# Kernel optimization log

Measured on AMD Instinct MI355X. Metric: run time of the kernel, lower is better.

Reference implementation:

```python
import jax, jax.numpy as jnp
import numpy as np

ALPHA = 0.5  # init alpha
B, T, D, H = 32, 1024, 512, 512


def _cell(x, h, c, wih, whh, bih, bhh):
    # PyTorch LSTM cell: gates in i, f, g, o order
    g = x @ wih.T + bih + h @ whh.T + bhh  # (B, 4H)
    i, f, gg, o = jnp.split(g, 4, axis=-1)
    c2 = jax.nn.sigmoid(f) * c + jax.nn.sigmoid(i) * jnp.tanh(gg)
    h2 = jax.nn.sigmoid(o) * jnp.tanh(c2)
    return h2, c2


def setup_inputs() -> dict:
    key = jax.random.key(0)
    ks = jax.random.split(key, 9)
    s = 1.0 / np.sqrt(H)  # torch default init scale
    u = lambda k, shp: jax.random.uniform(k, shp, jnp.float32, -s, s)
    return {
        "u_sequence": jax.random.normal(ks[0], (B, T, D), jnp.float32),
        "w_ih_f": u(ks[1], (4 * H, D)),
        "w_hh_f": u(ks[2], (4 * H, H)),
        "b_ih_f": u(ks[3], (4 * H,)),
        "b_hh_f": u(ks[4], (4 * H,)),
        "w_ih_b": u(ks[5], (4 * H, D)),
        "w_hh_b": u(ks[6], (4 * H, H)),
        "b_ih_b": u(ks[7], (4 * H,)),
        "b_hh_b": u(ks[8], (4 * H,)),
    }


def reference(u_sequence, w_ih_f, w_hh_f, b_ih_f, b_hh_f,
              w_ih_b, w_hh_b, b_ih_b, b_hh_b):
    # Per timestep the original calls the bidirectional LSTM on a length-1
    # slice: both directions reduce to a single cell step on the same input.
    # Hidden/cell state (2, B, H) is carried across timesteps.
    pf = (w_ih_f, w_hh_f, b_ih_f, b_hh_f)
    pb = (w_ih_b, w_hh_b, b_ih_b, b_hh_b)
    Bn, Tn, Dn = u_sequence.shape
    Hn = w_hh_f.shape[1]
    z = jnp.zeros((Bn, Hn), u_sequence.dtype)

    def bi_step(x, hf, cf, hb, cb):
        hf2, cf2 = _cell(x, hf, cf, *pf)
        hb2, cb2 = _cell(x, hb, cb, *pb)
        # lstm_out[:, 0, :] == concat(h_fwd, h_bwd) for seq_len == 1
        return jnp.concatenate([hf2, hb2], axis=-1), hf2, cf2, hb2, cb2

    def step(carry, u_t):  # u_t: (B, D)
        hf, cf, hb, cb = carry
        out1, hf1, cf1, hb1, cb1 = bi_step(u_t, hf, cf, hb, cb)
        x_hat = out1[:, -1:]                 # last channel scalar, (B, 1)
        x_hat_prime = u_t + x_hat            # broadcast -> (B, D)
        out2, hf2, cf2, hb2, cb2 = bi_step(x_hat_prime, hf1, cf1, hb1, cb1)
        x_hat_next = out2[:, -1:]
        out = u_t + (1.0 - ALPHA) * x_hat_prime + ALPHA * x_hat_next
        return (hf2, cf2, hb2, cb2), out

    u_tm = jnp.swapaxes(u_sequence, 0, 1)    # (T, B, D)
    _, outs = jax.lax.scan(step, (z, z, z, z), u_tm)
    return jnp.swapaxes(outs, 0, 1)          # (B, T, D)
```

## Files before the change

kernel.cpp:

```cpp
#include <hip/hip_runtime.h>
#include <cstdint>
#include <cstddef>

#define BB 32
#define TT 1024
#define DD 512
#define HH 512
#define NBLK 128

typedef __bf16 bf16x8 __attribute__((ext_vector_type(8)));
typedef float  f32x4  __attribute__((ext_vector_type(4)));
typedef unsigned long long u64;

#define HFRAG_OFF 0
#define XHAT_OFF  131072
#define XS_OFF    393216
#define FLAGS_OFF 655360

#define AT_LOAD(p)     __hip_atomic_load((p),      __ATOMIC_RELAXED, __HIP_MEMORY_SCOPE_AGENT)
#define AT_STORE(p, v) __hip_atomic_store((p), (v), __ATOMIC_RELAXED, __HIP_MEMORY_SCOPE_AGENT)

__device__ __forceinline__ float sigm(float x) {
    return 1.f / (1.f + __expf(-x));
}
__device__ __forceinline__ float tanh_fast(float x) {
    x = fminf(15.f, fmaxf(-15.f, x));
    float e = __expf(2.f * x);
    return (e - 1.f) / (e + 1.f);
}

__device__ __forceinline__ void barrier_arrive(int* flags, int bid, int n) {
    __builtin_amdgcn_s_waitcnt(0);
    __syncthreads();
    if (threadIdx.x == 0) AT_STORE(&flags[bid], n);
}
__device__ __forceinline__ void barrier_wait(const int* flags, int dir, int n) {
    if (threadIdx.x < 64) {
        const u64* f64 = (const u64*)(flags + (dir << 6));
        const int i = threadIdx.x & 31;
        for (;;) {
            u64 a = AT_LOAD(&f64[i]);
            bool ok = ((int)a >= n) & ((int)(a >> 32) >= n);
            if (__all(ok)) break;
            __builtin_amdgcn_s_sleep(1);
        }
    }
    __syncthreads();
}

__global__ __launch_bounds__(256, 1) void lstm_persistent(
    const float* __restrict__ u,
    const float* __restrict__ wih_f, const float* __restrict__ whh_f,
    const float* __restrict__ bih_f, const float* __restrict__ bhh_f,
    const float* __restrict__ wih_b, const float* __restrict__ whh_b,
    const float* __restrict__ bih_b, const float* __restrict__ bhh_b,
    unsigned short* __restrict__ hfrag, float* __restrict__ xhat,
    u64* __restrict__ xs, int* __restrict__ flags)
{
    const int bid  = blockIdx.x;
    const int dir  = bid >> 6;
    const int kb   = bid & 63;
    const int k0   = kb << 3;
    const int tid  = threadIdx.x;
    const int wid  = tid >> 6;
    const int mi   = wid >> 1;
    const int ni   = wid & 1;
    const int lane = tid & 63;
    const int quad = lane >> 4;
    const int l16  = lane & 15;

    const float* wih = dir ? wih_b : wih_f;
    const float* whh = dir ? whh_b : whh_f;
    const float* bih = dir ? bih_b : bih_f;
    const float* bhh = dir ? bhh_b : bhh_f;

    bf16x8 wihF[16], whhF[16];
    {
        const int jg = (l16 >> 2) * HH + (k0 + 4 * mi) + (l16 & 3);
        #pragma unroll
        for (int s = 0; s < 16; ++s) {
            const float* p = wih + (size_t)jg * DD + s * 32 + quad * 8;
            const float* q = whh + (size_t)jg * HH + s * 32 + quad * 8;
            bf16x8 a, b;
            #pragma unroll
            for (int i = 0; i < 8; ++i) { a[i] = (__bf16)p[i]; b[i] = (__bf16)q[i]; }
            wihF[s] = a;
            whhF[s] = b;
        }
    }

    const int kc = k0 + 4 * mi + quad;
    const int bc = ni * 16 + l16;

    float rsv[4], biasv[4];
    {
        float rs = 0.f;
        #pragma unroll
        for (int s = 0; s < 16; ++s)
            #pragma unroll
            for (int i = 0; i < 8; ++i) rs += (float)wihF[s][i];
        rs += __shfl_xor(rs, 16);
        rs += __shfl_xor(rs, 32);
        #pragma unroll
        for (int g = 0; g < 4; ++g) {
            rsv[g]   = __shfl(rs, g * 4 + quad);
            const int j = g * HH + kc;
            biasv[g] = bih[j] + bhh[j];
        }
    }

    const int sw = kc >> 5, qw = (kc >> 3) & 3, iw = kc & 7;
    const int lanew = qw * 16 + l16;
    unsigned* hfrag32 = (unsigned*)hfrag;
    const int ws32_0 = (((((dir * 2 + 0) * 2 + ni) * 16 + sw) * 64 + lanew) * 8 + iw) >> 1;
    const int ws32_1 = ws32_0 + (2 * 16 * 64 * 8 >> 1);
    const u64* h64 = (const u64*)hfrag;
    const int rbA = ((dir * 2 + 0) * 2 + ni) * 2048 + lane * 2;
    const int rbB = ((dir * 2 + 1) * 2 + ni) * 2048 + lane * 2;

    if (!(quad & 1)) AT_STORE(&hfrag32[ws32_0], 0u);

    __shared__ __align__(16) float gbuf[4][16][20];

    auto ugemm = [&](int t) -> f32x4 {
        f32x4 a0 = (f32x4){0.f, 0.f, 0.f, 0.f};
        f32x4 a1 = (f32x4){0.f, 0.f, 0.f, 0.f};
        const float* ub = u + (size_t)bc * (TT * DD) + (size_t)t * DD + quad * 8;
        #pragma unroll
        for (int s = 0; s < 16; ++s) {
            const float4* p = (const float4*)(ub + s * 32);
            float4 x0 = p[0], x1 = p[1];
            bf16x8 uf;
            uf[0] = (__bf16)x0.x; uf[1] = (__bf16)x0.y;
            uf[2] = (__bf16)x0.z; uf[3] = (__bf16)x0.w;
            uf[4] = (__bf16)x1.x; uf[5] = (__bf16)x1.y;
            uf[6] = (__bf16)x1.z; uf[7] = (__bf16)x1.w;
            if (s & 1) a1 = __builtin_amdgcn_mfma_f32_16x16x32_bf16(wihF[s], uf, a1, 0, 0, 0);
            else       a0 = __builtin_amdgcn_mfma_f32_16x16x32_bf16(wihF[s], uf, a0, 0, 0, 0);
        }
        return a0 + a1;
    };

    barrier_arrive(flags, bid, 1);
    f32x4 gih = ugemm(0);
    barrier_wait(flags, dir, 1);

    float c = 0.f;
    f32x4 gnext = gih;
    int n = 2;

    for (int t = 0; t < TT; ++t) {
        #pragma unroll 1
        for (int pass = 0; pass < 2; ++pass, ++n) {
            const int bufR = (t * 2 + pass) & 1;

            u64 ha[16], hb[16];
            {
                const int rb = bufR ? rbB : rbA;
                #pragma unroll
                for (int s = 0; s < 16; ++s) {
                    ha[s] = AT_LOAD(&h64[rb + s * 128]);
                    hb[s] = AT_LOAD(&h64[rb + s * 128 + 1]);
                }
            }
            f32x4 acc0 = gih;
            f32x4 acc1 = (f32x4){0.f, 0.f, 0.f, 0.f};
            #pragma unroll
            for (int s = 0; s < 16; ++s) {
                union { u64 q[2]; bf16x8 v; } cvt;
                cvt.q[0] = ha[s]; cvt.q[1] = hb[s];
                if (s & 1) acc1 = __builtin_amdgcn_mfma_f32_16x16x32_bf16(whhF[s], cvt.v, acc1, 0, 0, 0);
                else       acc0 = __builtin_amdgcn_mfma_f32_16x16x32_bf16(whhF[s], cvt.v, acc0, 0, 0, 0);
            }
            f32x4 acc = acc0 + acc1;

            float xc = 0.f;
            if (pass) {
                u64 v = AT_LOAD(&xs[t * BB + bc]);
                while ((int)(v >> 32) < 1) {
                    __builtin_amdgcn_s_sleep(1);
                    v = AT_LOAD(&xs[t * BB + bc]);
                }
                xc = __builtin_bit_cast(float, (unsigned)v);
            }

            float4 gw; gw.x = acc[0]; gw.y = acc[1]; gw.z = acc[2]; gw.w = acc[3];
            *(float4*)&gbuf[wid][l16][quad * 4] = gw;
            __syncthreads();
            float gI = gbuf[wid][l16][ 0 + quad] + biasv[0] + xc * rsv[0];
            float gF = gbuf[wid][l16][ 4 + quad] + biasv[1] + xc * rsv[1];
            float gG = gbuf[wid][l16][ 8 + quad] + biasv[2] + xc * rsv[2];
            float gO = gbuf[wid][l16][12 + quad] + biasv[3] + xc * rsv[3];

            float ig = sigm(gI), fg = sigm(gF), gg = tanh_fast(gG), og = sigm(gO);
            c = fg * c + ig * gg;
            float h = og * tanh_fast(c);

            float hp = __shfl_xor(h, 16);
            if (dir == 1 && kc == (HH - 1)) {
                AT_STORE(&xhat[pass * (TT * BB) + t * BB + bc], h);
                if (pass == 0)
                    AT_STORE(&xs[t * BB + bc],
                             ((u64)1u << 32) | (u64)__builtin_bit_cast(unsigned, h));
            }
            if (!(quad & 1)) {
                unsigned lo = (unsigned)__builtin_bit_cast(unsigned short, (__bf16)h);
                unsigned hi = (unsigned)__builtin_bit_cast(unsigned short, (__bf16)hp);
                AT_STORE(&hfrag32[bufR ? ws32_0 : ws32_1], lo | (hi << 16));
            }

            barrier_arrive(flags, bid, n);
            if (pass == 1 && t + 1 < TT)
                gnext = ugemm(t + 1);
            barrier_wait(flags, dir, n);
        }
        gih = gnext;
    }
}

__global__ void epilogue(const float* __restrict__ u, const float* __restrict__ xhat,
                         float* __restrict__ out)
{
    const int i = blockIdx.x * blockDim.x + threadIdx.x;
    const float4 uv = ((const float4*)u)[i];
    const int bt = i >> 7;
    const int t = bt & (TT - 1);
    const int b = bt >> 10;
    const float s = 0.5f * (xhat[t * BB + b] + xhat[TT * BB + t * BB + b]);
    float4 o;
    o.x = 1.5f * uv.x + s;
    o.y = 1.5f * uv.y + s;
    o.z = 1.5f * uv.z + s;
    o.w = 1.5f * uv.w + s;
    ((float4*)out)[i] = o;
}

extern "C" void kernel_launch(void* const* d_in, const int* in_sizes, int n_in,
                              void* d_out, int out_size, void* d_ws, size_t ws_size,
                              hipStream_t stream) {
    const float* u     = (const float*)d_in[0];
    const float* wih_f = (const float*)d_in[1];
    const float* whh_f = (const float*)d_in[2];
    const float* bih_f = (const float*)d_in[3];
    const float* bhh_f = (const float*)d_in[4];
    const float* wih_b = (const float*)d_in[5];
    const float* whh_b = (const float*)d_in[6];
    const float* bih_b = (const float*)d_in[7];
    const float* bhh_b = (const float*)d_in[8];

    char* ws = (char*)d_ws;
    unsigned short* hfrag = (unsigned short*)(ws + HFRAG_OFF);
    float* xhat           = (float*)(ws + XHAT_OFF);
    u64* xs               = (u64*)(ws + XS_OFF);
    int* flags            = (int*)(ws + FLAGS_OFF);

    lstm_persistent<<<NBLK, 256, 0, stream>>>(
        u, wih_f, whh_f, bih_f, bhh_f, wih_b, whh_b, bih_b, bhh_b,
        hfrag, xhat, xs, flags);

    const int n4 = BB * TT * DD / 4;
    epilogue<<<n4 / 256, 256, 0, stream>>>(u, xhat, (float*)d_out);
}
```

Before: 15.68 ms.

## Replace grid flag barrier with step-tagged hidden-state words for dataflow sync

Removes the per-pass global arrive/wait barrier across blocks of each direction. Instead, each bf16 hidden-state pair is stored as a 64-bit word tagged with its step number, and consumers spin on the tags of the fragments they read. The block-level __syncthreads around the gate shuffle becomes a wave barrier, and the sleep in the xs spin is dropped. This cuts synchronization latency on the serial critical path. In exchange, hidden-state traffic doubles and correctness now depends on tag ordering and stale workspace contents across calls.

```diff
diff --git a/kernel.cpp b/kernel.cpp
--- a/kernel.cpp
+++ b/kernel.cpp
@@ -13,9 +13,8 @@
 typedef unsigned long long u64;
 
 #define HFRAG_OFF 0
-#define XHAT_OFF  131072
-#define XS_OFF    393216
-#define FLAGS_OFF 655360
+#define XHAT_OFF  262144
+#define XS_OFF    524288
 
 #define AT_LOAD(p)     __hip_atomic_load((p),      __ATOMIC_RELAXED, __HIP_MEMORY_SCOPE_AGENT)
 #define AT_STORE(p, v) __hip_atomic_store((p), (v), __ATOMIC_RELAXED, __HIP_MEMORY_SCOPE_AGENT)
@@ -29,24 +28,6 @@
     return (e - 1.f) / (e + 1.f);
 }
 
-__device__ __forceinline__ void barrier_arrive(int* flags, int bid, int n) {
-    __builtin_amdgcn_s_waitcnt(0);
-    __syncthreads();
-    if (threadIdx.x == 0) AT_STORE(&flags[bid], n);
-}
-__device__ __forceinline__ void barrier_wait(const int* flags, int dir, int n) {
-    if (threadIdx.x < 64) {
-        const u64* f64 = (const u64*)(flags + (dir << 6));
-        const int i = threadIdx.x & 31;
-        for (;;) {
-            u64 a = AT_LOAD(&f64[i]);
-            bool ok = ((int)a >= n) & ((int)(a >> 32) >= n);
-            if (__all(ok)) break;
-            __builtin_amdgcn_s_sleep(1);
-        }
-    }
-    __syncthreads();
-}
 
 __global__ __launch_bounds__(256, 1) void lstm_persistent(
     const float* __restrict__ u,
@@ -54,8 +35,8 @@
     const float* __restrict__ bih_f, const float* __restrict__ bhh_f,
     const float* __restrict__ wih_b, const float* __restrict__ whh_b,
     const float* __restrict__ bih_b, const float* __restrict__ bhh_b,
-    unsigned short* __restrict__ hfrag, float* __restrict__ xhat,
-    u64* __restrict__ xs, int* __restrict__ flags)
+    u64* __restrict__ hfrag, float* __restrict__ xhat,
+    u64* __restrict__ xs)
 {
     const int bid  = blockIdx.x;
     const int dir  = bid >> 6;
@@ -109,16 +90,13 @@
         }
     }
 
-    const int sw = kc >> 5, qw = (kc >> 3) & 3, iw = kc & 7;
-    const int lanew = qw * 16 + l16;
-    unsigned* hfrag32 = (unsigned*)hfrag;
-    const int ws32_0 = (((((dir * 2 + 0) * 2 + ni) * 16 + sw) * 64 + lanew) * 8 + iw) >> 1;
-    const int ws32_1 = ws32_0 + (2 * 16 * 64 * 8 >> 1);
-    const u64* h64 = (const u64*)hfrag;
-    const int rbA = ((dir * 2 + 0) * 2 + ni) * 2048 + lane * 2;
-    const int rbB = ((dir * 2 + 1) * 2 + ni) * 2048 + lane * 2;
-
-    if (!(quad & 1)) AT_STORE(&hfrag32[ws32_0], 0u);
+    const int swq = kc >> 5, qw = (kc >> 3) & 3, pw = (kc & 7) >> 1;
+    const int wr0 = ((((dir * 2 + 0) * 2 + ni) * 16 + swq) * 64 + (qw * 16 + l16)) * 4 + pw;
+    const int wr1 = wr0 + 8192;
+    const int rb0 = ((dir * 2 + 0) * 2 + ni) * 4096;
+    const int rb1 = rb0 + 8192;
+
+    if (!(quad & 1)) AT_STORE(&hfrag[wr0], (u64)0);
 
     __shared__ __align__(16) float gbuf[4][16][20];
 
@@ -141,52 +119,59 @@
         return a0 + a1;
     };
 
-    barrier_arrive(flags, bid, 1);
     f32x4 gih = ugemm(0);
-    barrier_wait(flags, dir, 1);
-
+    f32x4 gnext = gih;
     float c = 0.f;
-    f32x4 gnext = gih;
-    int n = 2;
 
     for (int t = 0; t < TT; ++t) {
         #pragma unroll 1
-        for (int pass = 0; pass < 2; ++pass, ++n) {
-            const int bufR = (t * 2 + pass) & 1;
-
-            u64 ha[16], hb[16];
-            {
-                const int rb = bufR ? rbB : rbA;
+        for (int pass = 0; pass < 2; ++pass) {
+            const int g  = 2 * t + pass + 1;
+            const int st = g - 1;
+            const u64* rp = hfrag + ((g & 1) ? rb0 : rb1);
+
+            u64 hv[64];
+            #pragma unroll
+            for (int s = 0; s < 16; ++s)
                 #pragma unroll
-                for (int s = 0; s < 16; ++s) {
-                    ha[s] = AT_LOAD(&h64[rb + s * 128]);
-                    hb[s] = AT_LOAD(&h64[rb + s * 128 + 1]);
-                }
-            }
+                for (int p = 0; p < 4; ++p)
+                    hv[s * 4 + p] = AT_LOAD(&rp[(s * 64 + lane) * 4 + p]);
+
             f32x4 acc0 = gih;
             f32x4 acc1 = (f32x4){0.f, 0.f, 0.f, 0.f};
             #pragma unroll
             for (int s = 0; s < 16; ++s) {
-                union { u64 q[2]; bf16x8 v; } cvt;
-                cvt.q[0] = ha[s]; cvt.q[1] = hb[s];
-                if (s & 1) acc1 = __builtin_amdgcn_mfma_f32_16x16x32_bf16(whhF[s], cvt.v, acc1, 0, 0, 0);
-                else       acc0 = __builtin_amdgcn_mfma_f32_16x16x32_bf16(whhF[s], cvt.v, acc0, 0, 0, 0);
+                for (;;) {
+                    bool ok = ((int)(hv[s * 4 + 0] >> 32) == st) &
+                              ((int)(hv[s * 4 + 1] >> 32) == st) &
+                              ((int)(hv[s * 4 + 2] >> 32) == st) &
+                              ((int)(hv[s * 4 + 3] >> 32) == st);
+                    if (__all(ok)) break;
+                    #pragma unroll
+                    for (int p = 0; p < 4; ++p)
+                        hv[s * 4 + p] = AT_LOAD(&rp[(s * 64 + lane) * 4 + p]);
+                }
+                union { unsigned w[4]; bf16x8 v; } f;
+                f.w[0] = (unsigned)hv[s * 4 + 0];
+                f.w[1] = (unsigned)hv[s * 4 + 1];
+                f.w[2] = (unsigned)hv[s * 4 + 2];
+                f.w[3] = (unsigned)hv[s * 4 + 3];
+                if (s & 1) acc1 = __builtin_amdgcn_mfma_f32_16x16x32_bf16(whhF[s], f.v, acc1, 0, 0, 0);
+                else       acc0 = __builtin_amdgcn_mfma_f32_16x16x32_bf16(whhF[s], f.v, acc0, 0, 0, 0);
             }
             f32x4 acc = acc0 + acc1;
 
             float xc = 0.f;
             if (pass) {
                 u64 v = AT_LOAD(&xs[t * BB + bc]);
-                while ((int)(v >> 32) < 1) {
-                    __builtin_amdgcn_s_sleep(1);
+                while ((int)(v >> 32) < 1)
                     v = AT_LOAD(&xs[t * BB + bc]);
-                }
                 xc = __builtin_bit_cast(float, (unsigned)v);
             }
 
             float4 gw; gw.x = acc[0]; gw.y = acc[1]; gw.z = acc[2]; gw.w = acc[3];
             *(float4*)&gbuf[wid][l16][quad * 4] = gw;
-            __syncthreads();
+            __builtin_amdgcn_wave_barrier();
             float gI = gbuf[wid][l16][ 0 + quad] + biasv[0] + xc * rsv[0];
             float gF = gbuf[wid][l16][ 4 + quad] + biasv[1] + xc * rsv[1];
             float gG = gbuf[wid][l16][ 8 + quad] + biasv[2] + xc * rsv[2];
@@ -206,13 +191,12 @@
             if (!(quad & 1)) {
                 unsigned lo = (unsigned)__builtin_bit_cast(unsigned short, (__bf16)h);
                 unsigned hi = (unsigned)__builtin_bit_cast(unsigned short, (__bf16)hp);
-                AT_STORE(&hfrag32[bufR ? ws32_0 : ws32_1], lo | (hi << 16));
-            }
-
-            barrier_arrive(flags, bid, n);
+                u64 out = ((u64)(unsigned)g << 32) | (u64)(lo | (hi << 16));
+                AT_STORE(&hfrag[(g & 1) ? wr1 : wr0], out);
+            }
+
             if (pass == 1 && t + 1 < TT)
                 gnext = ugemm(t + 1);
-            barrier_wait(flags, dir, n);
         }
         gih = gnext;
     }
@@ -249,14 +233,13 @@
     const float* bhh_b = (const float*)d_in[8];
 
     char* ws = (char*)d_ws;
-    unsigned short* hfrag = (unsigned short*)(ws + HFRAG_OFF);
-    float* xhat           = (float*)(ws + XHAT_OFF);
-    u64* xs               = (u64*)(ws + XS_OFF);
-    int* flags            = (int*)(ws + FLAGS_OFF);
+    u64* hfrag  = (u64*)(ws + HFRAG_OFF);
+    float* xhat = (float*)(ws + XHAT_OFF);
+    u64* xs     = (u64*)(ws + XS_OFF);
 
     lstm_persistent<<<NBLK, 256, 0, stream>>>(
         u, wih_f, whh_f, bih_f, bhh_f, wih_b, whh_b, bih_b, bhh_b,
-        hfrag, xhat, xs, flags);
+        hfrag, xhat, xs);
 
     const int n4 = BB * TT * DD / 4;
     epilogue<<<n4 / 256, 256, 0, stream>>>(u, xhat, (float*)d_out);
```

Result: slower. 21.10 ms (+34.6%).
